# Kernel optimization log

Hardware: AMD Instinct MI355X
Metric: run time of the kernel (lower is better)

Reference implementation:

```python
import jax, jax.numpy as jnp
import numpy as np

DIM = 384
HEADS = 12
HEAD_DIM = DIM // HEADS
WS = 7          # window_size
SS = 3          # shift_size (SW-MSA)
DIM_FF = 4 * DIM
EPS = 1e-5


def _rel_pos_index():
    coords = np.stack(np.meshgrid(np.arange(WS), np.arange(WS), indexing='ij'))
    cf = coords.reshape(2, -1)                       # (2, 49)
    rel = cf[:, :, None] - cf[:, None, :]            # (2, 49, 49)
    rel = rel.transpose(1, 2, 0).astype(np.int64)
    rel[:, :, 0] += WS - 1
    rel[:, :, 1] += WS - 1
    rel[:, :, 0] *= 2 * WS - 1
    return rel.sum(-1)                               # (49, 49)


def _attn_mask(Hp, Wp):
    # cyclic-shift mask, computed on static shapes with numpy
    img = np.zeros((Hp, Wp))
    slices = (slice(0, -WS), slice(-WS, -SS), slice(-SS, None))
    cnt = 0
    for hs in slices:
        for ws_ in slices:
            img[hs, ws_] = cnt
            cnt += 1
    mw = img.reshape(Hp // WS, WS, Wp // WS, WS).transpose(0, 2, 1, 3).reshape(-1, WS * WS)
    am = mw[:, None, :] - mw[:, :, None]             # unsqueeze(1) - unsqueeze(2)
    am = np.where(am != 0, -100.0, 0.0)
    return jnp.asarray(am, jnp.float32)              # (nW, 49, 49)


def _ln(x, g, b):
    mu = jnp.mean(x, -1, keepdims=True)
    var = jnp.mean(jnp.square(x - mu), -1, keepdims=True)
    return (x - mu) * jax.lax.rsqrt(var + EPS) * g + b


def setup_inputs() -> dict:
    key = jax.random.key(0)
    ks = jax.random.split(key, 8)
    B, H, W = 32, 56, 56
    s = 0.02
    return {
        'x': jax.random.normal(ks[0], (B, H * W, DIM), jnp.float32),
        'H': H, 'W': W,
        'rel_idx': jnp.asarray(_rel_pos_index(), jnp.int32),
        'rpb_table': jax.random.normal(ks[1], ((2 * WS - 1) ** 2, HEADS), jnp.float32) * s,
        'qkv_w': jax.random.normal(ks[2], (DIM, 3 * DIM), jnp.float32) * s,
        'proj_w': jax.random.normal(ks[3], (DIM, DIM), jnp.float32) * s,
        'proj_b': jnp.zeros((DIM,), jnp.float32),
        'norm1_g': jnp.ones((DIM,), jnp.float32),
        'norm1_b': jnp.zeros((DIM,), jnp.float32),
        'norm2_g': jnp.ones((DIM,), jnp.float32),
        'norm2_b': jnp.zeros((DIM,), jnp.float32),
        'ffn_w1': jax.random.normal(ks[4], (DIM, DIM_FF), jnp.float32) * s,
        'ffn_b1': jnp.zeros((DIM_FF,), jnp.float32),
        'ffn_w2': jax.random.normal(ks[5], (DIM_FF, DIM), jnp.float32) * s,
        'ffn_b2': jnp.zeros((DIM,), jnp.float32),
    }


def reference(x, H, W, rel_idx, rpb_table, qkv_w, proj_w, proj_b,
              norm1_g, norm1_b, norm2_g, norm2_b,
              ffn_w1, ffn_b1, ffn_w2, ffn_b2):
    B, L, C = x.shape
    shortcut = x
    h = _ln(x, norm1_g, norm1_b).reshape(B, H, W, C)

    pad_b = (WS - H % WS) % WS
    pad_r = (WS - W % WS) % WS
    if pad_b > 0 or pad_r > 0:
        h = jnp.pad(h, ((0, 0), (0, pad_b), (0, pad_r), (0, 0)))
    Hp, Wp = H + pad_b, W + pad_r

    if SS > 0:
        h = jnp.roll(h, (-SS, -SS), axis=(1, 2))

    # window partition -> (B*nW, 49, C)
    nHw, nWw = Hp // WS, Wp // WS
    win = h.reshape(B, nHw, WS, nWw, WS, C).transpose(0, 1, 3, 2, 4, 5)
    win = win.reshape(-1, WS * WS, C)
    Bw, N = win.shape[0], WS * WS

    # window attention
    qkv = (win @ qkv_w).reshape(Bw, N, 3, HEADS, HEAD_DIM)
    q, k, v = [qkv[:, :, i].transpose(0, 2, 1, 3) for i in range(3)]  # (Bw, heads, N, hd)
    attn = jnp.einsum('bhnd,bhmd->bhnm', q, k) / np.sqrt(HEAD_DIM)

    bias = rpb_table[rel_idx]                      # (N, N, heads)
    attn = attn + bias.transpose(2, 0, 1)[None]

    if SS > 0:
        mask = _attn_mask(Hp, Wp)                  # (nW, N, N)
        nW = mask.shape[0]
        attn = attn.reshape(B, nW, HEADS, N, N) + mask[None, :, None]
        attn = attn.reshape(Bw, HEADS, N, N)

    attn = jax.nn.softmax(attn, axis=-1)
    out = jnp.einsum('bhnm,bhmd->bnhd', attn, v).reshape(Bw, N, C)
    out = out @ proj_w + proj_b

    # window reverse
    out = out.reshape(B, nHw, nWw, WS, WS, C).transpose(0, 1, 3, 2, 4, 5)
    out = out.reshape(B, Hp, Wp, C)
    if SS > 0:
        out = jnp.roll(out, (SS, SS), axis=(1, 2))
    if pad_b > 0 or pad_r > 0:
        out = out[:, :H, :W, :]

    h = shortcut + out.reshape(B, H * W, C)
    ff = _ln(h, norm2_g, norm2_b)
    ff = jax.nn.gelu(ff @ ffn_w1 + ffn_b1, approximate=False) @ ffn_w2 + ffn_b2
    return h + ff
```

## Files before the change

kernel.cpp:

```cpp
#include <hip/hip_runtime.h>

#define DEV __device__ __forceinline__

typedef __bf16 bf16x8 __attribute__((ext_vector_type(8)));
typedef float  f32x4  __attribute__((ext_vector_type(4)));
typedef unsigned short u16x8 __attribute__((ext_vector_type(8)));
typedef unsigned short u16x4 __attribute__((ext_vector_type(4)));
typedef long  longx2 __attribute__((ext_vector_type(2)));

DEV float b2f(unsigned short u) {
    unsigned int t = ((unsigned int)u) << 16;
    return __uint_as_float(t);
}
DEV unsigned short f2b(float f) {
    unsigned int u = __float_as_uint(f);
    unsigned int r = (u + 0x7FFFu + ((u >> 16) & 1u)) >> 16;
    return (unsigned short)r;
}
DEV unsigned char f2f8(float f) {
    return (unsigned char)(__builtin_amdgcn_cvt_pk_fp8_f32(f, f, 0, false) & 0xff);
}

DEV int kpos(int c) {
    int s = (c >> 3) & 7;
    return (c & ~63) | ((((s & 3) << 1) | (s >> 2)) << 3) | (c & 7);
}

DEV void gload_lds16(const void* g, void* l) {
    __builtin_amdgcn_global_load_lds(
        (const __attribute__((address_space(1))) void*)g,
        (__attribute__((address_space(3))) void*)l, 16, 0, 0);
}

DEV size_t win_to_tok(int row) {
    int w = row / 49, t = row - w * 49;
    int b  = w >> 6, widx = w & 63;
    int wi = widx >> 3, wj = widx & 7;
    int ti = t / 7, tj = t - ti * 7;
    int hh = wi * 7 + ti + 3; if (hh >= 56) hh -= 56;
    int ww = wj * 7 + tj + 3; if (ww >= 56) ww -= 56;
    return (size_t)b * 3136 + (size_t)hh * 56 + ww;
}

__global__ void tokmap_build(int* __restrict__ tm, int T) {
    int i = blockIdx.x * 256 + threadIdx.x;
    if (i < T) tm[i] = (int)win_to_tok(i);
}

__global__ void wprep8(const float* __restrict__ src, unsigned char* __restrict__ dst,
                       int K, int N) {
    int idx = blockIdx.x * 256 + threadIdx.x;
    if (idx >= K * N) return;
    int k = idx / N, n = idx - k * N;
    dst[(size_t)n * K + kpos(k)] = f2f8(src[idx]);
}

__global__ void btab_build(const int* __restrict__ rel_idx, const float* __restrict__ rpb,
                           float* __restrict__ tab) {
    int idx = blockIdx.x * 256 + threadIdx.x;
    if (idx >= 4 * 12 * 64 * 64) return;
    int col = idx & 63, row = (idx >> 6) & 63;
    int h = (idx >> 12) % 12, cls = idx / (12 * 4096);
    float v;
    if (row >= 49 || col >= 49) {
        v = -10000.f;
    } else {
        v = rpb[rel_idx[row * 49 + col] * 12 + h];
        int ti = row / 7, tj = row - (row / 7) * 7;
        int si = col / 7, sj = col - (col / 7) * 7;
        int lq = ((cls & 2) ? (ti < 4 ? 1 : 2) : 0) * 3 + ((cls & 1) ? (tj < 4 ? 1 : 2) : 0);
        int lk = ((cls & 2) ? (si < 4 ? 1 : 2) : 0) * 3 + ((cls & 1) ? (sj < 4 ? 1 : 2) : 0);
        if (lq != lk) v -= 100.f;
    }
    tab[idx] = v;
}

template <int REMAP>
__global__ __launch_bounds__(256) void ln_kernel(const float* __restrict__ x,
                                                 const float* __restrict__ g,
                                                 const float* __restrict__ b,
                                                 unsigned char* __restrict__ out,
                                                 int rows) {
    int r = blockIdx.x * 4 + (threadIdx.x >> 6);
    int lane = threadIdx.x & 63;
    if (r >= rows) return;
    size_t src = REMAP ? win_to_tok(r) : (size_t)r;
    const float* xp = x + src * 384;
    float v[6];
    float s = 0.f;
#pragma unroll
    for (int i = 0; i < 6; ++i) { v[i] = xp[i * 64 + lane]; s += v[i]; }
#pragma unroll
    for (int off = 32; off; off >>= 1) s += __shfl_xor(s, off, 64);
    float mu = s * (1.f / 384.f);
    float q = 0.f;
#pragma unroll
    for (int i = 0; i < 6; ++i) { float d = v[i] - mu; q += d * d; }
#pragma unroll
    for (int off = 32; off; off >>= 1) q += __shfl_xor(q, off, 64);
    float inv = rsqrtf(q * (1.f / 384.f) + 1e-5f);
    unsigned char* op = out + (size_t)r * 384;
#pragma unroll
    for (int i = 0; i < 6; ++i) {
        int c = i * 64 + lane;
        op[kpos(c)] = f2f8((v[i] - mu) * inv * g[c] + b[c]);
    }
}

template <int MODE, int NBUF, int DEPTH, int SB, int MINW>
__global__ __launch_bounds__(256, MINW) void gemm_f8_kernel(const unsigned char* __restrict__ A,
                                                            const unsigned char* __restrict__ Bt,
                                                            int M, int N, int K,
                                                            const float* __restrict__ bias,
                                                            const float* __restrict__ resid,
                                                            const int* __restrict__ tokmap,
                                                            unsigned char* __restrict__ outb8,
                                                            float* __restrict__ outf) {
    static_assert(SB ? (NBUF >= DEPTH + 2) : (NBUF >= DEPTH + 1), "ring too small");
    __shared__ unsigned char As[NBUF][128 * 64];
    __shared__ unsigned char Bs[NBUF][128 * 64];
    const int tid = threadIdx.x;
    const int wid = tid >> 6, lane = tid & 63;
    const int ntile = N >> 7;

    int bid = blockIdx.x;
    int nwg = gridDim.x;
    int swb = ((nwg & 7) == 0) ? ((bid & 7) * (nwg >> 3) + (bid >> 3)) : bid;
    const int mt = swb / ntile, nt = swb - mt * ntile;
    const int wr = wid >> 1, wc = wid & 1;

    f32x4 acc[4][4] = {};

    const unsigned char* Abase = A  + (size_t)(mt * 128) * K;
    const unsigned char* Bbase = Bt + (size_t)(nt * 128) * K;

    auto stage = [&](int buf, int k0) {
#pragma unroll
        for (int j = 0; j < 2; ++j) {
            int r  = j * 64 + (tid >> 2);
            int gp = (tid & 3) ^ ((r >> 1) & 3);
            gload_lds16(Abase + (size_t)r * K + k0 + gp * 16, &As[buf][j * 4096 + tid * 16]);
            gload_lds16(Bbase + (size_t)r * K + k0 + gp * 16, &Bs[buf][j * 4096 + tid * 16]);
        }
    };

    const int fr = lane & 15, kq = lane >> 4;
    const int rowA = wr * 64 + fr;
    const int rowB = wc * 64 + fr;
    const int cb = (kq ^ ((fr >> 1) & 3)) << 4;

    const int nk = K >> 6;
    stage(0, 0);
    if (DEPTH >= 2 && nk > 1) stage(1, 64);

    for (int t = 0; t < nk; ++t) {
        const int cur = t % NBUF;
        if (t + DEPTH < nk) {
            stage((t + DEPTH) % NBUF, (t + DEPTH) << 6);
            if constexpr (DEPTH == 1) {
                asm volatile("s_waitcnt vmcnt(4)" ::: "memory");
            } else {
                asm volatile("s_waitcnt vmcnt(8)" ::: "memory");
            }
        } else if (DEPTH >= 2 && t + 1 < nk) {
            asm volatile("s_waitcnt vmcnt(4)" ::: "memory");
        } else {
            asm volatile("s_waitcnt vmcnt(0)" ::: "memory");
        }
        __builtin_amdgcn_s_barrier();

        longx2 a[4], b[4];
#pragma unroll
        for (int m = 0; m < 4; ++m)
            a[m] = *(const longx2*)(&As[cur][(rowA + m * 16) * 64 + cb]);
#pragma unroll
        for (int n = 0; n < 4; ++n)
            b[n] = *(const longx2*)(&Bs[cur][(rowB + n * 16) * 64 + cb]);
#pragma unroll
        for (int ks = 0; ks < 2; ++ks)
#pragma unroll
            for (int m = 0; m < 4; ++m)
#pragma unroll
                for (int n = 0; n < 4; ++n)
                    acc[m][n] = __builtin_amdgcn_mfma_f32_16x16x32_fp8_fp8(b[n][ks], a[m][ks], acc[m][n], 0, 0, 0);

        asm volatile("s_waitcnt lgkmcnt(0)" ::: "memory");
        if constexpr (SB == 0) __builtin_amdgcn_s_barrier();
    }

    const int row0 = mt * 128 + wr * 64;
    const int col0 = nt * 128 + wc * 64;
    const int rl = lane & 15;
    const int cq = (lane >> 4) << 2;
#pragma unroll
    for (int m = 0; m < 4; ++m) {
        int row = row0 + m * 16 + rl;
        size_t tok = 0;
        if constexpr (MODE == 1) tok = (size_t)tokmap[row];
#pragma unroll
        for (int n = 0; n < 4; ++n) {
            int col = col0 + n * 16 + cq;
            f32x4 v = acc[m][n];
            if constexpr (MODE == 0) {
                int pk = 0;
                pk = __builtin_amdgcn_cvt_pk_fp8_f32(v[0], v[1], pk, false);
                pk = __builtin_amdgcn_cvt_pk_fp8_f32(v[2], v[3], pk, true);
                *(int*)(outb8 + (size_t)row * N + col) = pk;
            } else if constexpr (MODE == 1) {
                size_t o = tok * 384 + col;
                f32x4 rv = *(const f32x4*)&resid[o];
                f32x4 bb = *(const f32x4*)&bias[col];
                f32x4 ov = rv + v + bb;
                *(f32x4*)&outf[o] = ov;
            } else if constexpr (MODE == 2) {
                f32x4 bb = *(const f32x4*)&bias[col];
                float g4[4];
#pragma unroll
                for (int r = 0; r < 4; ++r) {
                    float t2 = v[r] + bb[r];
                    float e  = __expf(-1.702f * t2);
                    g4[r] = t2 * __builtin_amdgcn_rcpf(1.f + e);
                }
                int pk = 0;
                pk = __builtin_amdgcn_cvt_pk_fp8_f32(g4[0], g4[1], pk, false);
                pk = __builtin_amdgcn_cvt_pk_fp8_f32(g4[2], g4[3], pk, true);
                *(int*)(outb8 + (size_t)row * N + kpos(col)) = pk;
            } else {
                size_t o = (size_t)row * N + col;
                f32x4 rv = *(const f32x4*)&resid[o];
                f32x4 bb = *(const f32x4*)&bias[col];
                f32x4 ov = rv + v + bb;
                *(f32x4*)&outf[o] = ov;
            }
        }
    }
}

__global__ __launch_bounds__(256, 2) void attn_kernel(const unsigned char* __restrict__ QKV8,
                                                      const float* __restrict__ Btab,
                                                      unsigned char* __restrict__ O8) {
    __shared__ char lds[8192 + 16384 + 32768];
    char* Kl = lds;
    char* Vl = lds + 8192;
    char* Pl = lds + 24576;

    const int w   = blockIdx.x;
    const int tid = threadIdx.x, wid = tid >> 6, lane = tid & 63;
    const int fr  = lane & 15, kq = lane >> 4;
    const size_t base = (size_t)w * 49 * 1152;
    const int widx = w & 63, wi = widx >> 3, wj = widx & 7;
    const int cls = ((wi == 7) ? 2 : 0) | ((wj == 7) ? 1 : 0);
    const float* tb = Btab + (size_t)cls * 12 * 4096;
    constexpr float SCL = 0.17677669529663687f;

    for (int R = 0; R < 3; ++R) {
        if (R) __syncthreads();
        {
            f32x4 z = {};
#pragma unroll
            for (int j = 0; j < 6; ++j) *(f32x4*)(lds + j * 4096 + tid * 16) = z;
        }
        __syncthreads();
        {
            int hh = tid >> 6, h = R * 4 + hh;
#pragma unroll
            for (int it = 0; it < 4; ++it) {
                int i = (tid & 63) + it * 64;
                if (i < 196) {
                    int m = i >> 2, c = i & 3;
                    long k8 = *(const long*)(QKV8 + base + (size_t)m * 1152 + 384 + h * 32 + c * 8);
                    int s = c ^ (m & 3) ^ ((m >> 2) & 3);
                    *(long*)(Kl + hh * 2048 + m * 32 + s * 8) = k8;
                    long v8 = *(const long*)(QKV8 + base + (size_t)m * 1152 + 768 + h * 32 + c * 8);
                    int lo = (int)v8, hi = (int)(v8 >> 32);
                    float vf[8];
                    vf[0] = __builtin_amdgcn_cvt_f32_fp8(lo, 0);
                    vf[1] = __builtin_amdgcn_cvt_f32_fp8(lo, 1);
                    vf[2] = __builtin_amdgcn_cvt_f32_fp8(lo, 2);
                    vf[3] = __builtin_amdgcn_cvt_f32_fp8(lo, 3);
                    vf[4] = __builtin_amdgcn_cvt_f32_fp8(hi, 0);
                    vf[5] = __builtin_amdgcn_cvt_f32_fp8(hi, 1);
                    vf[6] = __builtin_amdgcn_cvt_f32_fp8(hi, 2);
                    vf[7] = __builtin_amdgcn_cvt_f32_fp8(hi, 3);
#pragma unroll
                    for (int j = 0; j < 8; ++j) {
                        int d = c * 8 + j;
                        *(unsigned short*)(Vl + hh * 4096 + d * 128 +
                                           (((m >> 3) ^ (d & 7)) * 16) + (m & 7) * 2) = f2b(vf[j]);
                    }
                }
            }
        }
        __syncthreads();

        const int h = R * 4 + wid;
        const float* tbh = tb + h * 4096;

        long aq[4], bk[4];
#pragma unroll
        for (int mi = 0; mi < 4; ++mi) {
            int row = mi * 16 + fr; if (row > 48) row = 48;
            aq[mi] = *(const long*)(QKV8 + base + (size_t)row * 1152 + h * 32 + kq * 8);
        }
#pragma unroll
        for (int ni = 0; ni < 4; ++ni) {
            int rk = ni * 16 + fr;
            bk[ni] = *(const long*)(Kl + wid * 2048 + rk * 32 +
                                    ((kq ^ (rk & 3) ^ ((rk >> 2) & 3)) * 8));
        }
        f32x4 s[4][4] = {};
#pragma unroll
        for (int mi = 0; mi < 4; ++mi)
#pragma unroll
            for (int ni = 0; ni < 4; ++ni)
                s[mi][ni] = __builtin_amdgcn_mfma_f32_16x16x32_fp8_fp8(bk[ni], aq[mi], s[mi][ni], 0, 0, 0);

        float linv_[4];
#pragma unroll
        for (int mi = 0; mi < 4; ++mi) {
            int row = mi * 16 + fr;
            const float* tr = tbh + row * 64 + kq * 4;
            f32x4 sv[4];
            float mx = -1e30f;
#pragma unroll
            for (int ni = 0; ni < 4; ++ni) {
                f32x4 bb = *(const f32x4*)&tr[ni * 16];
                sv[ni] = s[mi][ni] * SCL + bb;
                mx = fmaxf(mx, fmaxf(fmaxf(sv[ni][0], sv[ni][1]), fmaxf(sv[ni][2], sv[ni][3])));
            }
            mx = fmaxf(mx, __shfl_xor(mx, 16, 64));
            mx = fmaxf(mx, __shfl_xor(mx, 32, 64));
            float sm = 0.f;
#pragma unroll
            for (int ni = 0; ni < 4; ++ni)
#pragma unroll
                for (int r = 0; r < 4; ++r) { sv[ni][r] = __expf(sv[ni][r] - mx); sm += sv[ni][r]; }
            sm += __shfl_xor(sm, 16, 64);
            sm += __shfl_xor(sm, 32, 64);
            linv_[mi] = __builtin_amdgcn_rcpf(sm);
#pragma unroll
            for (int ni = 0; ni < 4; ++ni) {
                int colb = ni * 16 + kq * 4;
                int phys = (colb >> 3) ^ (row & 7);
                u16x4 pk;
#pragma unroll
                for (int r = 0; r < 4; ++r) pk[r] = f2b(sv[ni][r]);
                *(u16x4*)(Pl + wid * 8192 + row * 128 + phys * 16 + (colb & 7) * 2) = pk;
            }
        }
        asm volatile("s_waitcnt lgkmcnt(0)" ::: "memory");
        __builtin_amdgcn_sched_barrier(0);

        f32x4 oacc[4][2] = {};
#pragma unroll
        for (int sl = 0; sl < 2; ++sl) {
            bf16x8 bv[2];
#pragma unroll
            for (int ni = 0; ni < 2; ++ni) {
                int d = ni * 16 + fr;
                bv[ni] = *(const bf16x8*)(Vl + wid * 4096 + d * 128 + (((sl * 4 + kq) ^ (d & 7)) * 16));
            }
#pragma unroll
            for (int mi = 0; mi < 4; ++mi) {
                int row = mi * 16 + fr;
                bf16x8 ap = *(const bf16x8*)(Pl + wid * 8192 + row * 128 + (((sl * 4 + kq) ^ (row & 7)) * 16));
#pragma unroll
                for (int ni = 0; ni < 2; ++ni)
                    oacc[mi][ni] = __builtin_amdgcn_mfma_f32_16x16x32_bf16(bv[ni], ap, oacc[mi][ni], 0, 0, 0);
            }
        }

#pragma unroll
        for (int mi = 0; mi < 4; ++mi) {
            int row = mi * 16 + fr;
            if (row < 49) {
                float li = linv_[mi];
                unsigned char* opb = O8 + (size_t)(w * 49 + row) * 384;
#pragma unroll
                for (int ni = 0; ni < 2; ++ni) {
                    int c = h * 32 + ni * 16 + kq * 4;
                    int pk = 0;
                    pk = __builtin_amdgcn_cvt_pk_fp8_f32(oacc[mi][ni][0] * li, oacc[mi][ni][1] * li, pk, false);
                    pk = __builtin_amdgcn_cvt_pk_fp8_f32(oacc[mi][ni][2] * li, oacc[mi][ni][3] * li, pk, true);
                    *(int*)(opb + kpos(c)) = pk;
                }
            }
        }
    }
}

extern "C" void kernel_launch(void* const* d_in, const int* in_sizes, int n_in,
                              void* d_out, int out_size, void* d_ws, size_t ws_size,
                              hipStream_t stream) {
    const float* x     = (const float*)d_in[0];
    const int*   rel   = (const int*)  d_in[3];
    const float* rpb   = (const float*)d_in[4];
    const float* qkvw  = (const float*)d_in[5];
    const float* projw = (const float*)d_in[6];
    const float* projb = (const float*)d_in[7];
    const float* n1g   = (const float*)d_in[8];
    const float* n1b   = (const float*)d_in[9];
    const float* n2g   = (const float*)d_in[10];
    const float* n2b   = (const float*)d_in[11];
    const float* w1    = (const float*)d_in[12];
    const float* b1    = (const float*)d_in[13];
    const float* w2    = (const float*)d_in[14];
    const float* b2    = (const float*)d_in[15];
    float* out = (float*)d_out;

    const int T = in_sizes[0] / 384;

    char* ws = (char*)d_ws;
    size_t off = 0;
    auto alloc = [&](size_t bytes) {
        char* p = ws + off;
        off += (bytes + 255) & ~(size_t)255;
        return p;
    };
    unsigned char* Wq8  = (unsigned char*)alloc((size_t)1152 * 384);
    unsigned char* Wp8  = (unsigned char*)alloc((size_t)384 * 384);
    unsigned char* W18  = (unsigned char*)alloc((size_t)1536 * 384);
    unsigned char* W28  = (unsigned char*)alloc((size_t)384 * 1536);
    float*         Btab = (float*)       alloc((size_t)4 * 12 * 4096 * 4);
    int*           Tmap = (int*)         alloc((size_t)T * 4);
    unsigned char* slotA = (unsigned char*)alloc((size_t)T * 384);
    unsigned char* slotB = (unsigned char*)alloc((size_t)T * 1536);

    unsigned char* X1   = slotA;
    unsigned char* O8   = slotA;
    unsigned char* X2   = slotA;
    unsigned char* QKV8 = slotB;
    unsigned char* F8   = slotB;
    float*         Hh   = out;

    wprep8<<<dim3((1152 * 384 + 255) / 256), 256, 0, stream>>>(qkvw, Wq8, 384, 1152);
    wprep8<<<dim3((384 * 384 + 255) / 256),  256, 0, stream>>>(projw, Wp8, 384, 384);
    wprep8<<<dim3((384 * 1536 + 255) / 256), 256, 0, stream>>>(w1, W18, 384, 1536);
    wprep8<<<dim3((1536 * 384 + 255) / 256), 256, 0, stream>>>(w2, W28, 1536, 384);
    btab_build<<<dim3((4 * 12 * 4096 + 255) / 256), 256, 0, stream>>>(rel, rpb, Btab);
    tokmap_build<<<dim3((T + 255) / 256), 256, 0, stream>>>(Tmap, T);

    ln_kernel<1><<<dim3(T / 4), 256, 0, stream>>>(x, n1g, n1b, X1, T);
    gemm_f8_kernel<0, 2, 1, 0, 4><<<dim3((T / 128) * (1152 / 128)), 256, 0, stream>>>(
        X1, Wq8, T, 1152, 384, nullptr, nullptr, nullptr, QKV8, nullptr);
    attn_kernel<<<dim3(T / 49), 256, 0, stream>>>(QKV8, Btab, O8);
    gemm_f8_kernel<1, 2, 1, 0, 4><<<dim3((T / 128) * (384 / 128)), 256, 0, stream>>>(
        O8, Wp8, T, 384, 384, projb, x, Tmap, nullptr, Hh);
    ln_kernel<0><<<dim3(T / 4), 256, 0, stream>>>(Hh, n2g, n2b, X2, T);
    gemm_f8_kernel<2, 2, 1, 0, 4><<<dim3((T / 128) * (1536 / 128)), 256, 0, stream>>>(
        X2, W18, T, 1536, 384, b1, nullptr, nullptr, F8, nullptr);
    gemm_f8_kernel<3, 4, 2, 1, 2><<<dim3((T / 128) * (384 / 128)), 256, 0, stream>>>(
        F8, W28, T, 384, 1536, b2, Hh, nullptr, nullptr, out);
}
```

Before: 662.1 us.

## Load full K=384 into LDS for K=384 GEMMs with 64x128 tiles

For the three GEMMs whose K is 384, a new kernel loads the whole A (64 rows) and B (128 rows) K-slab into LDS up front with a single wait and barrier. It then runs all six k-steps with no per-step barriers, each wave owning a 64x32 output slice. This removes the per-iteration sync and pipeline bookkeeping and doubles the grid size. The cost is 72KB of LDS per block and no overlap of loads with MFMA inside a block. The FFN2 GEMM keeps the ring-buffer pipeline in a specialised kernel.

```diff
diff --git a/kernel.cpp b/kernel.cpp
--- a/kernel.cpp
+++ b/kernel.cpp
@@ -107,18 +107,17 @@
     }
 }
 
-template <int MODE, int NBUF, int DEPTH, int SB, int MINW>
-__global__ __launch_bounds__(256, MINW) void gemm_f8_kernel(const unsigned char* __restrict__ A,
-                                                            const unsigned char* __restrict__ Bt,
-                                                            int M, int N, int K,
-                                                            const float* __restrict__ bias,
-                                                            const float* __restrict__ resid,
-                                                            const int* __restrict__ tokmap,
-                                                            unsigned char* __restrict__ outb8,
-                                                            float* __restrict__ outf) {
-    static_assert(SB ? (NBUF >= DEPTH + 2) : (NBUF >= DEPTH + 1), "ring too small");
-    __shared__ unsigned char As[NBUF][128 * 64];
-    __shared__ unsigned char Bs[NBUF][128 * 64];
+template <int MODE>
+__global__ __launch_bounds__(256, 2) void gemm_f8_fullk(const unsigned char* __restrict__ A,
+                                                        const unsigned char* __restrict__ Bt,
+                                                        int M, int N, int K,
+                                                        const float* __restrict__ bias,
+                                                        const float* __restrict__ resid,
+                                                        const int* __restrict__ tokmap,
+                                                        unsigned char* __restrict__ outb8,
+                                                        float* __restrict__ outf) {
+    __shared__ unsigned char Als[64 * 384];
+    __shared__ unsigned char Bls[128 * 384];
     const int tid = threadIdx.x;
     const int wid = tid >> 6, lane = tid & 63;
     const int ntile = N >> 7;
@@ -127,69 +126,53 @@
     int nwg = gridDim.x;
     int swb = ((nwg & 7) == 0) ? ((bid & 7) * (nwg >> 3) + (bid >> 3)) : bid;
     const int mt = swb / ntile, nt = swb - mt * ntile;
-    const int wr = wid >> 1, wc = wid & 1;
-
-    f32x4 acc[4][4] = {};
-
-    const unsigned char* Abase = A  + (size_t)(mt * 128) * K;
+
+    const unsigned char* Abase = A  + (size_t)(mt * 64) * K;
     const unsigned char* Bbase = Bt + (size_t)(nt * 128) * K;
 
-    auto stage = [&](int buf, int k0) {
-#pragma unroll
-        for (int j = 0; j < 2; ++j) {
-            int r  = j * 64 + (tid >> 2);
-            int gp = (tid & 3) ^ ((r >> 1) & 3);
-            gload_lds16(Abase + (size_t)r * K + k0 + gp * 16, &As[buf][j * 4096 + tid * 16]);
-            gload_lds16(Bbase + (size_t)r * K + k0 + gp * 16, &Bs[buf][j * 4096 + tid * 16]);
-        }
-    };
+    {
+        int rA = tid >> 2;
+        int gpA = (tid & 3) ^ ((rA >> 1) & 3);
+#pragma unroll
+        for (int kb = 0; kb < 6; ++kb)
+            gload_lds16(Abase + (size_t)rA * K + kb * 64 + gpA * 16, &Als[kb * 4096 + tid * 16]);
+#pragma unroll
+        for (int kb = 0; kb < 6; ++kb)
+#pragma unroll
+            for (int j = 0; j < 2; ++j) {
+                int r = j * 64 + (tid >> 2);
+                int gp = (tid & 3) ^ ((r >> 1) & 3);
+                gload_lds16(Bbase + (size_t)r * K + kb * 64 + gp * 16,
+                            &Bls[kb * 8192 + j * 4096 + tid * 16]);
+            }
+    }
+    asm volatile("s_waitcnt vmcnt(0)" ::: "memory");
+    __builtin_amdgcn_s_barrier();
 
     const int fr = lane & 15, kq = lane >> 4;
-    const int rowA = wr * 64 + fr;
-    const int rowB = wc * 64 + fr;
     const int cb = (kq ^ ((fr >> 1) & 3)) << 4;
 
-    const int nk = K >> 6;
-    stage(0, 0);
-    if (DEPTH >= 2 && nk > 1) stage(1, 64);
-
-    for (int t = 0; t < nk; ++t) {
-        const int cur = t % NBUF;
-        if (t + DEPTH < nk) {
-            stage((t + DEPTH) % NBUF, (t + DEPTH) << 6);
-            if constexpr (DEPTH == 1) {
-                asm volatile("s_waitcnt vmcnt(4)" ::: "memory");
-            } else {
-                asm volatile("s_waitcnt vmcnt(8)" ::: "memory");
-            }
-        } else if (DEPTH >= 2 && t + 1 < nk) {
-            asm volatile("s_waitcnt vmcnt(4)" ::: "memory");
-        } else {
-            asm volatile("s_waitcnt vmcnt(0)" ::: "memory");
-        }
-        __builtin_amdgcn_s_barrier();
-
-        longx2 a[4], b[4];
+    f32x4 acc[4][2] = {};
+#pragma unroll
+    for (int kb = 0; kb < 6; ++kb) {
+        longx2 a[4], b[2];
 #pragma unroll
         for (int m = 0; m < 4; ++m)
-            a[m] = *(const longx2*)(&As[cur][(rowA + m * 16) * 64 + cb]);
-#pragma unroll
-        for (int n = 0; n < 4; ++n)
-            b[n] = *(const longx2*)(&Bs[cur][(rowB + n * 16) * 64 + cb]);
+            a[m] = *(const longx2*)(&Als[kb * 4096 + (m * 16 + fr) * 64 + cb]);
+#pragma unroll
+        for (int n = 0; n < 2; ++n)
+            b[n] = *(const longx2*)(&Bls[kb * 8192 + (wid * 32 + n * 16 + fr) * 64 + cb]);
 #pragma unroll
         for (int ks = 0; ks < 2; ++ks)
 #pragma unroll
             for (int m = 0; m < 4; ++m)
 #pragma unroll
-                for (int n = 0; n < 4; ++n)
+                for (int n = 0; n < 2; ++n)
                     acc[m][n] = __builtin_amdgcn_mfma_f32_16x16x32_fp8_fp8(b[n][ks], a[m][ks], acc[m][n], 0, 0, 0);
-
-        asm volatile("s_waitcnt lgkmcnt(0)" ::: "memory");
-        if constexpr (SB == 0) __builtin_amdgcn_s_barrier();
-    }
-
-    const int row0 = mt * 128 + wr * 64;
-    const int col0 = nt * 128 + wc * 64;
+    }
+
+    const int row0 = mt * 64;
+    const int col0 = nt * 128 + wid * 32;
     const int rl = lane & 15;
     const int cq = (lane >> 4) << 2;
 #pragma unroll
@@ -198,7 +181,7 @@
         size_t tok = 0;
         if constexpr (MODE == 1) tok = (size_t)tokmap[row];
 #pragma unroll
-        for (int n = 0; n < 4; ++n) {
+        for (int n = 0; n < 2; ++n) {
             int col = col0 + n * 16 + cq;
             f32x4 v = acc[m][n];
             if constexpr (MODE == 0) {
@@ -212,7 +195,7 @@
                 f32x4 bb = *(const f32x4*)&bias[col];
                 f32x4 ov = rv + v + bb;
                 *(f32x4*)&outf[o] = ov;
-            } else if constexpr (MODE == 2) {
+            } else {
                 f32x4 bb = *(const f32x4*)&bias[col];
                 float g4[4];
 #pragma unroll
@@ -225,13 +208,101 @@
                 pk = __builtin_amdgcn_cvt_pk_fp8_f32(g4[0], g4[1], pk, false);
                 pk = __builtin_amdgcn_cvt_pk_fp8_f32(g4[2], g4[3], pk, true);
                 *(int*)(outb8 + (size_t)row * N + kpos(col)) = pk;
-            } else {
-                size_t o = (size_t)row * N + col;
-                f32x4 rv = *(const f32x4*)&resid[o];
-                f32x4 bb = *(const f32x4*)&bias[col];
-                f32x4 ov = rv + v + bb;
-                *(f32x4*)&outf[o] = ov;
-            }
+            }
+        }
+    }
+}
+
+template <int NBUF, int DEPTH, int MINW>
+__global__ __launch_bounds__(256, MINW) void gemm_f8_ring(const unsigned char* __restrict__ A,
+                                                          const unsigned char* __restrict__ Bt,
+                                                          int M, int N, int K,
+                                                          const float* __restrict__ bias,
+                                                          const float* __restrict__ resid,
+                                                          float* __restrict__ outf) {
+    static_assert(NBUF >= DEPTH + 2, "ring too small");
+    __shared__ unsigned char As[NBUF][128 * 64];
+    __shared__ unsigned char Bs[NBUF][128 * 64];
+    const int tid = threadIdx.x;
+    const int wid = tid >> 6, lane = tid & 63;
+    const int ntile = N >> 7;
+
+    int bid = blockIdx.x;
+    int nwg = gridDim.x;
+    int swb = ((nwg & 7) == 0) ? ((bid & 7) * (nwg >> 3) + (bid >> 3)) : bid;
+    const int mt = swb / ntile, nt = swb - mt * ntile;
+    const int wr = wid >> 1, wc = wid & 1;
+
+    f32x4 acc[4][4] = {};
+
+    const unsigned char* Abase = A  + (size_t)(mt * 128) * K;
+    const unsigned char* Bbase = Bt + (size_t)(nt * 128) * K;
+
+    auto stage = [&](int buf, int k0) {
+#pragma unroll
+        for (int j = 0; j < 2; ++j) {
+            int r  = j * 64 + (tid >> 2);
+            int gp = (tid & 3) ^ ((r >> 1) & 3);
+            gload_lds16(Abase + (size_t)r * K + k0 + gp * 16, &As[buf][j * 4096 + tid * 16]);
+            gload_lds16(Bbase + (size_t)r * K + k0 + gp * 16, &Bs[buf][j * 4096 + tid * 16]);
+        }
+    };
+
+    const int fr = lane & 15, kq = lane >> 4;
+    const int rowA = wr * 64 + fr;
+    const int rowB = wc * 64 + fr;
+    const int cb = (kq ^ ((fr >> 1) & 3)) << 4;
+
+    const int nk = K >> 6;
+    stage(0, 0);
+    if (nk > 1) stage(1, 64);
+
+    for (int t = 0; t < nk; ++t) {
+        const int cur = t % NBUF;
+        if (t + DEPTH < nk) {
+            stage((t + DEPTH) % NBUF, (t + DEPTH) << 6);
+            asm volatile("s_waitcnt vmcnt(8)" ::: "memory");
+        } else if (t + 1 < nk) {
+            asm volatile("s_waitcnt vmcnt(4)" ::: "memory");
+        } else {
+            asm volatile("s_waitcnt vmcnt(0)" ::: "memory");
+        }
+        __builtin_amdgcn_s_barrier();
+
+        longx2 a[4], b[4];
+#pragma unroll
+        for (int m = 0; m < 4; ++m)
+            a[m] = *(const longx2*)(&As[cur][(rowA + m * 16) * 64 + cb]);
+#pragma unroll
+        for (int n = 0; n < 4; ++n)
+            b[n] = *(const longx2*)(&Bs[cur][(rowB + n * 16) * 64 + cb]);
+#pragma unroll
+        for (int ks = 0; ks < 2; ++ks)
+#pragma unroll
+            for (int m = 0; m < 4; ++m)
+#pragma unroll
+                for (int n = 0; n < 4; ++n)
+                    acc[m][n] = __builtin_amdgcn_mfma_f32_16x16x32_fp8_fp8(b[n][ks], a[m][ks], acc[m][n], 0, 0, 0);
+
+        asm volatile("s_waitcnt lgkmcnt(0)" ::: "memory");
+    }
+
+    const int row0 = mt * 128 + wr * 64;
+    const int col0 = nt * 128 + wc * 64;
+    const int rl = lane & 15;
+    const int cq = (lane >> 4) << 2;
+#pragma unroll
+    for (int m = 0; m < 4; ++m) {
+        int row = row0 + m * 16 + rl;
+#pragma unroll
+        for (int n = 0; n < 4; ++n) {
+            int col = col0 + n * 16 + cq;
+            f32x4 v = acc[m][n];
+            size_t o = (size_t)row * N + col;
+            f32x4 rv = *(const f32x4*)&resid[o];
+            f32x4 bb = *(const f32x4*)&bias[col];
+            f32x4 ov = rv + v + bb;
+            *(f32x4*)&outf[o] = ov;
         }
     }
 }
@@ -441,14 +512,14 @@
     tokmap_build<<<dim3((T + 255) / 256), 256, 0, stream>>>(Tmap, T);
 
     ln_kernel<1><<<dim3(T / 4), 256, 0, stream>>>(x, n1g, n1b, X1, T);
-    gemm_f8_kernel<0, 2, 1, 0, 4><<<dim3((T / 128) * (1152 / 128)), 256, 0, stream>>>(
+    gemm_f8_fullk<0><<<dim3((T / 64) * (1152 / 128)), 256, 0, stream>>>(
         X1, Wq8, T, 1152, 384, nullptr, nullptr, nullptr, QKV8, nullptr);
     attn_kernel<<<dim3(T / 49), 256, 0, stream>>>(QKV8, Btab, O8);
-    gemm_f8_kernel<1, 2, 1, 0, 4><<<dim3((T / 128) * (384 / 128)), 256, 0, stream>>>(
+    gemm_f8_fullk<1><<<dim3((T / 64) * (384 / 128)), 256, 0, stream>>>(
         O8, Wp8, T, 384, 384, projb, x, Tmap, nullptr, Hh);
     ln_kernel<0><<<dim3(T / 4), 256, 0, stream>>>(Hh, n2g, n2b, X2, T);
-    gemm_f8_kernel<2, 2, 1, 0, 4><<<dim3((T / 128) * (1536 / 128)), 256, 0, stream>>>(
+    gemm_f8_fullk<2><<<dim3((T / 64) * (1536 / 128)), 256, 0, stream>>>(
         X2, W18, T, 1536, 384, b1, nullptr, nullptr, F8, nullptr);
-    gemm_f8_kernel<3, 4, 2, 1, 2><<<dim3((T / 128) * (384 / 128)), 256, 0, stream>>>(
-        F8, W28, T, 384, 1536, b2, Hh, nullptr, nullptr, out);
-}
+    gemm_f8_ring<4, 2, 2><<<dim3((T / 128) * (384 / 128)), 256, 0, stream>>>(
+        F8, W28, T, 384, 1536, b2, Hh, out);
+}
```

Measured after the change: 656.4 us. About the same (-0.9%).
